# Kernel optimization log

Hardware: AMD Instinct MI355X
Metric: run time of the kernel (lower is better)

## Reference

```python
import jax, jax.numpy as jnp
import numpy as np
from jax import lax

FEAT_STRIDE = 16
SCALES = (8, 16, 32)
RATIOS = (0.5, 1.0, 2.0)
PRE_NMS = 6000
POST_NMS = 300
NMS_THRESH = 0.7
MIN_SIZE = 16.0


def _base_anchors():
    base = 16.0
    cx = cy = base / 2.0
    anchors = []
    for r in RATIOS:
        for s in SCALES:
            h = base * s * np.sqrt(r)
            w = base * s * np.sqrt(1.0 / r)
            anchors.append([cx - w / 2, cy - h / 2, cx + w / 2, cy + h / 2])
    return np.asarray(anchors, np.float32)  # [A,4] (x1,y1,x2,y2)


def _shifted_anchors(h, w):
    base = _base_anchors()
    sy = np.arange(h, dtype=np.float32) * FEAT_STRIDE
    sx = np.arange(w, dtype=np.float32) * FEAT_STRIDE
    yy, xx = np.meshgrid(sy, sx, indexing='ij')  # h-major then w, matching NHWC permute
    shifts = np.stack([xx, yy, xx, yy], axis=-1).reshape(-1, 1, 4)
    return (shifts + base[None]).reshape(-1, 4).astype(np.float32)  # [h*w*A,4]


def _conv(x, w, b, pad):
    y = lax.conv_general_dilated(x, w, (1, 1), [(pad, pad), (pad, pad)],
                                 dimension_numbers=('NCHW', 'OIHW', 'NCHW'))
    return y + b[None, :, None, None]


def _iou(box, boxes):
    lt = jnp.maximum(box[:2], boxes[:, :2])
    rb = jnp.minimum(box[2:], boxes[:, 2:])
    wh = jnp.maximum(rb - lt, 0.0)
    inter = wh[:, 0] * wh[:, 1]
    a1 = (box[2] - box[0]) * (box[3] - box[1])
    a2 = (boxes[:, 2] - boxes[:, 0]) * (boxes[:, 3] - boxes[:, 1])
    return inter / (a1 + a2 - inter + 1e-9)


def _nms_proposals(boxes, scores):
    # boxes [K,4], scores [K] -> [POST_NMS,4]
    ws = boxes[:, 2] - boxes[:, 0]
    hs = boxes[:, 3] - boxes[:, 1]
    scores = jnp.where((ws >= MIN_SIZE) & (hs >= MIN_SIZE), scores, -jnp.inf)
    top_s, idx = lax.top_k(scores, PRE_NMS)
    b = boxes[idx]

    def body(i, st):
        keep, s = st
        j = jnp.argmax(s).astype(jnp.int32)
        keep = keep.at[i].set(j)
        sup = _iou(b[j], b) >= NMS_THRESH  # suppresses j itself too (iou=1)
        s = jnp.where(sup, -jnp.inf, s)
        return keep, s

    keep, _ = lax.fori_loop(0, POST_NMS, body,
                            (jnp.zeros((POST_NMS,), jnp.int32), top_s))
    return b[keep]


def setup_inputs() -> dict:
    key = jax.random.key(0)
    ks = jax.random.split(key, 5)
    n, c, h, w = 8, 512, 50, 64
    A = len(SCALES) * len(RATIOS)
    x = jax.random.normal(ks[0], (n, c, h, w), jnp.float32)
    w1 = jax.random.normal(ks[1], (512, 512, 3, 3), jnp.float32) * 0.02
    b1 = jnp.zeros((512,), jnp.float32)
    w_cls = jax.random.normal(ks[2], (A * 2, 512, 1, 1), jnp.float32) * 0.02
    b_cls = jnp.zeros((A * 2,), jnp.float32)
    w_bbox = jax.random.normal(ks[3], (A * 4, 512, 1, 1), jnp.float32) * 0.005
    b_bbox = jnp.zeros((A * 4,), jnp.float32)
    return {'x': x, 'w1': w1, 'b1': b1, 'w_cls': w_cls, 'b_cls': b_cls,
            'w_bbox': w_bbox, 'b_bbox': b_bbox}


def reference(x, w1, b1, w_cls, b_cls, w_bbox, b_bbox):
    n, _, h, w = x.shape
    A = len(SCALES) * len(RATIOS)
    img_h, img_w = h * FEAT_STRIDE, w * FEAT_STRIDE
    anchors = jnp.asarray(_shifted_anchors(h, w))  # [h*w*A,4]

    feat = jax.nn.relu(_conv(x, w1, b1, 1))
    cls = _conv(feat, w_cls, b_cls, 0).transpose(0, 2, 3, 1).reshape(n, h, w, A, 2)
    fg = jax.nn.softmax(cls, axis=-1)[..., 1].reshape(n, -1)  # [n, h*w*A]
    deltas = _conv(feat, w_bbox, b_bbox, 0).transpose(0, 2, 3, 1).reshape(n, -1, 4)

    # decode deltas against anchors
    aw = anchors[:, 2] - anchors[:, 0]
    ah = anchors[:, 3] - anchors[:, 1]
    acx = anchors[:, 0] + 0.5 * aw
    acy = anchors[:, 1] + 0.5 * ah
    cx = deltas[..., 0] * aw + acx
    cy = deltas[..., 1] * ah + acy
    pw = jnp.exp(deltas[..., 2]) * aw
    ph = jnp.exp(deltas[..., 3]) * ah
    boxes = jnp.stack([cx - 0.5 * pw, cy - 0.5 * ph,
                       cx + 0.5 * pw, cy + 0.5 * ph], axis=-1)  # [n,K,4]
    hi = jnp.asarray([img_w, img_h, img_w, img_h], jnp.float32)
    boxes = jnp.clip(boxes, 0.0, hi)

    rois = jax.vmap(_nms_proposals)(boxes, fg)  # [n,POST_NMS,4]
    roi_indices = jnp.repeat(jnp.arange(n, dtype=jnp.int32), POST_NMS)
    return rois.reshape(-1, 4), roi_indices
```

## Files before the change

kernel.cpp:

```cpp
#include <hip/hip_runtime.h>
#include <math.h>

#define NIMG 8
#define CIN  512
#define HF   50
#define WF   64
#define HW   3200
#define NA   9
#define KPER 28800
#define PRE  6000
#define POST 300

#define WHT_ELEMS  32768

#define NW    94
#define NCAP  6016
#define NTRI  4465

#define XTROWS 52
#define XTCOLS 66
#define XT_ELEMS ((size_t)NIMG * XTROWS * XTCOLS * CIN)
#define XT_BYTES (XT_ELEMS * 2)

#define WPK_ELEMS ((size_t)2 * 4 * 9 * 16 * 4096)
#define WPK_HALF  (4 * 9 * 16 * 4096)

#define SCALE_X 256.0f
#define SCALE_W 16384.0f
#define INV_SCALE (1.0f / 4194304.0f)

#define PB_XT   1600
#define PB_HALO 64
#define PB_WPK  288
#define PB_PH   16
#define PB_TOT  (PB_XT + PB_HALO + PB_WPK + PB_PH)

#define HALO_VPI 14848
#define HALO_TOT (NIMG * HALO_VPI)

typedef _Float16 f16x8 __attribute__((ext_vector_type(8)));
typedef float f32x4  __attribute__((ext_vector_type(4)));
typedef unsigned short u16x8 __attribute__((ext_vector_type(8)));
typedef unsigned long long u64;

__constant__ float BASEA[9][4] = {
  {-82.509667991878083f, -37.254833995939042f,  98.509667991878083f,  53.254833995939042f},
  {-173.01933598375617f, -82.509667991878083f, 189.01933598375617f,   98.509667991878083f},
  {-354.03867196751233f, -173.01933598375617f, 370.03867196751233f,  189.01933598375617f},
  { -56.0f,  -56.0f,  72.0f,  72.0f},
  {-120.0f, -120.0f, 136.0f, 136.0f},
  {-248.0f, -248.0f, 264.0f, 264.0f},
  {-37.254833995939042f, -82.509667991878083f,  53.254833995939042f,  98.509667991878083f},
  {-82.509667991878083f, -173.01933598375617f,  98.509667991878083f, 189.01933598375617f},
  {-173.01933598375617f, -354.03867196751233f, 189.01933598375617f,  370.03867196751233f},
};

__device__ __forceinline__ unsigned int ordf(float f) {
  unsigned int u = __float_as_uint(f);
  return (u & 0x80000000u) ? ~u : (u | 0x80000000u);
}

__device__ __forceinline__ unsigned short f2h(float f) {
  union { _Float16 h; unsigned short u; } cv;
  cv.h = (_Float16)f;
  return cv.u;
}
__device__ __forceinline__ float h2f(unsigned short u) {
  union { _Float16 h; unsigned short u; } cv;
  cv.u = u;
  return (float)cv.h;
}

__global__ __launch_bounds__(256) void k_prep_all(
    const float4* __restrict__ x4,
    const float* __restrict__ w1,
    const float* __restrict__ wc, const float* __restrict__ bc,
    const float* __restrict__ wb, const float* __restrict__ bb,
    unsigned short* __restrict__ xh, unsigned short* __restrict__ xl,
    unsigned short* __restrict__ wpk,
    float* __restrict__ WHT2, float* __restrict__ bh) {
  __shared__ float tile[128][65];
  const int blk = blockIdx.x;
  const int t = threadIdx.x;

  if (blk < PB_XT) {
    const int cic = blk & 3;
    const int rest = blk >> 2;
    const int hrow = rest % 50;
    const int n = rest / 50;
#pragma unroll
    for (int jj = 0; jj < 8; ++jj) {
      const int e = t + 256 * jj;
      const int row = e >> 4, c4 = e & 15;
      const float4 v = x4[(((size_t)(n * CIN + cic * 128 + row) * HF + hrow) << 4) + c4];
      tile[row][c4 * 4 + 0] = v.x;
      tile[row][c4 * 4 + 1] = v.y;
      tile[row][c4 * 4 + 2] = v.z;
      tile[row][c4 * 4 + 3] = v.w;
    }
    __syncthreads();
#pragma unroll
    for (int jj = 0; jj < 4; ++jj) {
      const int e = t + 256 * jj;
      const int w = e >> 4, c8 = e & 15;
      const size_t base = ((size_t)((n * XTROWS + (hrow + 1)) * XTCOLS) + (w + 1)) * CIN
                          + cic * 128 + c8 * 8;
      u16x8 hv, lv;
#pragma unroll
      for (int u = 0; u < 8; ++u) {
        const float g = tile[c8 * 8 + u][w] * SCALE_X;
        const unsigned short hh = f2h(g);
        hv[u] = (short)hh;
        lv[u] = (short)f2h(g - h2f(hh));
      }
      *reinterpret_cast<u16x8*>(xh + base) = hv;
      *reinterpret_cast<u16x8*>(xl + base) = lv;
    }
  } else if (blk < PB_XT + PB_HALO) {
    const u16x8 z = {0, 0, 0, 0, 0, 0, 0, 0};
    const int tid = (blk - PB_XT) * 256 + t;
    for (int v = tid; v < HALO_TOT; v += PB_HALO * 256) {
      const int n = v / HALO_VPI;
      const int r = v - n * HALO_VPI;
      int row, col, v8;
      if (r < 8448) {
        row = (r < 4224) ? 0 : 51;
        const int r2 = (r < 4224) ? r : r - 4224;
        col = r2 >> 6;
        v8 = r2 & 63;
      } else {
        const int q = r - 8448;
        row = 1 + (q >> 7);
        const int rr = q & 127;
        col = (rr >= 64) ? 65 : 0;
        v8 = rr & 63;
      }
      const size_t off = ((size_t)((n * XTROWS + row) * XTCOLS) + col) * CIN + v8 * 8;
      *reinterpret_cast<u16x8*>(xh + off) = z;
      *reinterpret_cast<u16x8*>(xl + off) = z;
    }
  } else if (blk < PB_XT + PB_HALO + PB_WPK) {
    const int tot = (int)WPK_ELEMS;
    const int tid = (blk - PB_XT - PB_HALO) * 256 + t;
    for (int idx = tid; idx < tot; idx += PB_WPK * 256) {
      const int i = idx & 4095;
      int rest = idx >> 12;
      const int ks = rest & 15; rest >>= 4;
      const int tap = rest % 9; rest /= 9;
      const int cob = rest & 3;
      const int sp = rest >> 2;
      const int col = i >> 5;
      const int slotp = (i >> 3) & 3;
      const int j = i & 7;
      const int s = slotp ^ ((col >> 1) & 3);
      const int ci = ks * 32 + s * 8 + j;
      const int co = cob * 128 + col;
      const float g = w1[((size_t)co * CIN + ci) * 9 + tap] * SCALE_W;
      const unsigned short hh = f2h(g);
      wpk[idx] = sp ? f2h(g - h2f(hh)) : hh;
    }
  } else {
    const int TOT = WHT_ELEMS + 64;
    const int tid = (blk - PB_XT - PB_HALO - PB_WPK) * 256 + t;
    for (int idx = tid; idx < TOT; idx += PB_PH * 256) {
      if (idx < WHT_ELEMS) {
        int r = idx & 3;
        int o = (idx >> 2) & 63;
        int c = (idx >> 8) * 4 + r;
        float v = 0.0f;
        if (o < 18) v = wc[(size_t)o * CIN + c];
        else if (o < 54) v = wb[(size_t)(o - 18) * CIN + c];
        WHT2[idx] = v;
      } else {
        int o = idx - WHT_ELEMS;
        float v = 0.0f;
        if (o < 18) v = bc[o];
        else if (o < 54) v = bb[o - 18];
        bh[o] = v;
      }
    }
  }
}

#define GLDS(gp, lp) __builtin_amdgcn_global_load_lds( \
    (const __attribute__((address_space(1))) unsigned int*)(gp), \
    (__attribute__((address_space(3))) unsigned int*)(lp), 16, 0, 0)

__global__ __launch_bounds__(256, 2) void k_convmfma(
    const unsigned short* __restrict__ xh,
    const unsigned short* __restrict__ xl,
    const unsigned short* __restrict__ wpk,
    const float* __restrict__ b1,
    float* __restrict__ feat) {
  __shared__ unsigned short lds[2][4][4096];

  const int raw = blockIdx.x;
  const int xcd = raw & 7;
  const int idx = raw >> 3;
  const int cob = xcd >> 1;
  const int pb  = (xcd & 1) * 100 + idx;

  const int n   = pb / 25;
  const int h0  = (pb - n * 25) * 2;
  const int t   = threadIdx.x;
  const int wid = t >> 6;
  const int l   = t & 63;
  const int wm  = wid >> 1;
  const int wn  = wid & 1;

  const int colp = l >> 2;
  const int sB = (((l & 3) ^ ((l >> 3) & 3)) << 3);
  const unsigned short* xsrc = (wid == 3) ? xl : xh;
  const size_t wA_base = (size_t)(wid & 1) * WPK_HALF;

  const int fr = l & 15;
  const int fq = l >> 4;
  const int slotr = ((fq ^ ((fr >> 1) & 3)) << 4);

  f32x4 acc[4][4] = {};

  auto stage = [&](int sbuf, int ti) {
    const int ks  = ti / 9;
    const int tap = ti - ks * 9;
    if (wid < 2) {
      const unsigned short* gp = wpk + wA_base
          + ((size_t)((cob * 9 + tap) * 16 + ks) << 12) + l * 8;
      unsigned short* lp = &lds[sbuf][wid][0];
#pragma unroll
      for (int q = 0; q < 8; ++q)
        GLDS(gp + q * 512, lp + q * 512);
    } else {
      const int ky = (tap * 11) >> 5;
      const int kx = tap - ky * 3;
      const size_t ebase = ((size_t)((n * XTROWS + h0 + ky) * XTCOLS + kx + colp) << 9)
                           + ks * 32 + sB;
      unsigned short* lp = &lds[sbuf][wid][0];
#pragma unroll
      for (int q = 0; q < 8; ++q)
        GLDS(xsrc + ebase + ((size_t)(((q >> 2) * XTCOLS + (q & 3) * 16)) << 9),
             lp + q * 512);
    }
  };

  stage(0, 0);
  __syncthreads();

  int buf = 0;
  for (int ti = 0; ti < 144; ++ti) {
    if (ti < 143) stage(buf ^ 1, ti + 1);

    f16x8 ah[4], al[4], bhf[4], blf[4];
#pragma unroll
    for (int mi = 0; mi < 4; ++mi) {
      const int off = (((wm << 6) + (mi << 4) + fr) << 6) + slotr;
      ah[mi] = *(const f16x8*)((const char*)&lds[buf][0][0] + off);
      al[mi] = *(const f16x8*)((const char*)&lds[buf][1][0] + off);
    }
#pragma unroll
    for (int ni = 0; ni < 4; ++ni) {
      const int off = (((wn << 6) + (ni << 4) + fr) << 6) + slotr;
      bhf[ni] = *(const f16x8*)((const char*)&lds[buf][2][0] + off);
      blf[ni] = *(const f16x8*)((const char*)&lds[buf][3][0] + off);
    }
#pragma unroll
    for (int mi = 0; mi < 4; ++mi)
#pragma unroll
      for (int ni = 0; ni < 4; ++ni) {
        acc[mi][ni] = __builtin_amdgcn_mfma_f32_16x16x32_f16(ah[mi], bhf[ni], acc[mi][ni], 0, 0, 0);
        acc[mi][ni] = __builtin_amdgcn_mfma_f32_16x16x32_f16(ah[mi], blf[ni], acc[mi][ni], 0, 0, 0);
        acc[mi][ni] = __builtin_amdgcn_mfma_f32_16x16x32_f16(al[mi], bhf[ni], acc[mi][ni], 0, 0, 0);
      }
    __syncthreads();
    buf ^= 1;
  }

  const int h = h0 + wn;
#pragma unroll
  for (int mi = 0; mi < 4; ++mi) {
    const int co = (cob << 7) + (wm << 6) + (mi << 4) + (fq << 2);
    const float4 bias = *(const float4*)&b1[co];
#pragma unroll
    for (int ni = 0; ni < 4; ++ni) {
      const int w = (ni << 4) + fr;
      float4 v;
      v.x = fmaxf(fmaf(acc[mi][ni][0], INV_SCALE, bias.x), 0.0f);
      v.y = fmaxf(fmaf(acc[mi][ni][1], INV_SCALE, bias.y), 0.0f);
      v.z = fmaxf(fmaf(acc[mi][ni][2], INV_SCALE, bias.z), 0.0f);
      v.w = fmaxf(fmaf(acc[mi][ni][3], INV_SCALE, bias.w), 0.0f);
      *(float4*)(feat + (((size_t)n * HW + h * WF + w) << 9) + co) = v;
    }
  }
}

__global__ __launch_bounds__(256) void k_head(const float* __restrict__ feat,
                                              const float* __restrict__ WHT2,
                                              const float* __restrict__ bh,
                                              float* __restrict__ scores,
                                              float4* __restrict__ boxes) {
  __shared__ float fsh[16][512];
  __shared__ float vsh[16][64];
  const int t = threadIdx.x;
  const int wvid = t >> 6;
  const int o = t & 63;
  const int pos0 = blockIdx.x * 16;

  {
    const float4* fsrc = reinterpret_cast<const float4*>(feat + ((size_t)pos0 << 9));
    float4* fdst = reinterpret_cast<float4*>(&fsh[0][0]);
#pragma unroll
    for (int i = 0; i < 8; ++i) fdst[t + 256 * i] = fsrc[t + 256 * i];
  }
  __syncthreads();

  {
    const int p0 = wvid * 4;
    float a0 = 0.f, a1 = 0.f, a2 = 0.f, a3 = 0.f;
    const float4* wp = reinterpret_cast<const float4*>(WHT2);
    const float4* f0 = reinterpret_cast<const float4*>(&fsh[p0 + 0][0]);
    const float4* f1 = reinterpret_cast<const float4*>(&fsh[p0 + 1][0]);
    const float4* f2 = reinterpret_cast<const float4*>(&fsh[p0 + 2][0]);
    const float4* f3 = reinterpret_cast<const float4*>(&fsh[p0 + 3][0]);
#pragma unroll 4
    for (int c4 = 0; c4 < 128; ++c4) {
      float4 w4 = wp[c4 * 64 + o];
      float4 v;
      v = f0[c4];
      a0 = fmaf(w4.x, v.x, a0); a0 = fmaf(w4.y, v.y, a0);
      a0 = fmaf(w4.z, v.z, a0); a0 = fmaf(w4.w, v.w, a0);
      v = f1[c4];
      a1 = fmaf(w4.x, v.x, a1); a1 = fmaf(w4.y, v.y, a1);
      a1 = fmaf(w4.z, v.z, a1); a1 = fmaf(w4.w, v.w, a1);
      v = f2[c4];
      a2 = fmaf(w4.x, v.x, a2); a2 = fmaf(w4.y, v.y, a2);
      a2 = fmaf(w4.z, v.z, a2); a2 = fmaf(w4.w, v.w, a2);
      v = f3[c4];
      a3 = fmaf(w4.x, v.x, a3); a3 = fmaf(w4.y, v.y, a3);
      a3 = fmaf(w4.z, v.z, a3); a3 = fmaf(w4.w, v.w, a3);
    }
    float bv = bh[o];
    vsh[p0 + 0][o] = a0 + bv;
    vsh[p0 + 1][o] = a1 + bv;
    vsh[p0 + 2][o] = a2 + bv;
    vsh[p0 + 3][o] = a3 + bv;
  }
  __syncthreads();

  if (t < 144) {
    const int p2 = t / 9, a = t % 9;
    const int pos = pos0 + p2;
    const int n = pos / HW;
    const int r = pos - n * HW;
    const int ph = r >> 6;
    const int pw = r & 63;

    float l0 = vsh[p2][a * 2];
    float l1 = vsh[p2][a * 2 + 1];
    float m  = fmaxf(l0, l1);
    float e0 = (float)exp((double)__fsub_rn(l0, m));
    float e1 = (float)exp((double)__fsub_rn(l1, m));
    float fg = __fdiv_rn(e1, __fadd_rn(e0, e1));

    float d0 = vsh[p2][18 + a * 4 + 0];
    float d1 = vsh[p2][18 + a * 4 + 1];
    float d2 = vsh[p2][18 + a * 4 + 2];
    float d3 = vsh[p2][18 + a * 4 + 3];

    float sx = (float)(pw * 16);
    float sy = (float)(ph * 16);
    float ax1 = __fadd_rn(BASEA[a][0], sx);
    float ay1 = __fadd_rn(BASEA[a][1], sy);
    float ax2 = __fadd_rn(BASEA[a][2], sx);
    float ay2 = __fadd_rn(BASEA[a][3], sy);
    float aw = __fsub_rn(ax2, ax1);
    float ah = __fsub_rn(ay2, ay1);
    float acx = __fadd_rn(ax1, __fmul_rn(0.5f, aw));
    float acy = __fadd_rn(ay1, __fmul_rn(0.5f, ah));
    float cx = __fadd_rn(__fmul_rn(d0, aw), acx);
    float cy = __fadd_rn(__fmul_rn(d1, ah), acy);
    float pwd = __fmul_rn((float)exp((double)d2), aw);
    float phd = __fmul_rn((float)exp((double)d3), ah);
    float x1 = __fsub_rn(cx, __fmul_rn(0.5f, pwd));
    float y1 = __fsub_rn(cy, __fmul_rn(0.5f, phd));
    float x2 = __fadd_rn(cx, __fmul_rn(0.5f, pwd));
    float y2 = __fadd_rn(cy, __fmul_rn(0.5f, phd));
    x1 = fminf(fmaxf(x1, 0.0f), 1024.0f);
    x2 = fminf(fmaxf(x2, 0.0f), 1024.0f);
    y1 = fminf(fmaxf(y1, 0.0f), 800.0f);
    y2 = fminf(fmaxf(y2, 0.0f), 800.0f);
    float wsz = __fsub_rn(x2, x1);
    float hsz = __fsub_rn(y2, y1);
    float sc = (wsz >= 16.0f && hsz >= 16.0f) ? fg : -__builtin_huge_valf();

    const int idx = n * KPER + r * NA + a;
    scores[idx] = sc;
    boxes[idx] = make_float4(x1, y1, x2, y2);
  }
}

__global__ __launch_bounds__(1024) void k_select(const float* __restrict__ scores,
                                                 const float4* __restrict__ boxes,
                                                 float4* __restrict__ sbox,
                                                 u64* __restrict__ valid) {
  __shared__ u64 sk[8192];
  __shared__ unsigned int whist[16][264];
  __shared__ unsigned int histT[256];
  __shared__ unsigned int sh_selB, sh_ngt, sh_binc, sh_num;
  const int n = blockIdx.x;
  const int t = threadIdx.x;
  const int wv = t >> 6;
  const float* sc = scores + (size_t)n * KPER;
  const float4* sc4 = reinterpret_cast<const float4*>(sc);

  for (int e = t; e < 8192; e += 1024) sk[e] = 0ull;

  unsigned int prefix = 0, prefMask = 0, ngt = 0, neq = 0;
  for (int shift = 24; shift >= 0; shift -= 8) {
    for (int e = t; e < 16 * 264; e += 1024) (&whist[0][0])[e] = 0u;
    __syncthreads();
    for (int i4 = t; i4 < KPER / 4; i4 += 1024) {
      const float4 v = sc4[i4];
      unsigned int u;
      u = ordf(v.x); if ((u & prefMask) == prefix) atomicAdd(&whist[wv][(u >> shift) & 255], 1u);
      u = ordf(v.y); if ((u & prefMask) == prefix) atomicAdd(&whist[wv][(u >> shift) & 255], 1u);
      u = ordf(v.z); if ((u & prefMask) == prefix) atomicAdd(&whist[wv][(u >> shift) & 255], 1u);
      u = ordf(v.w); if ((u & prefMask) == prefix) atomicAdd(&whist[wv][(u >> shift) & 255], 1u);
    }
    __syncthreads();
    if (t < 256) {
      unsigned int s = 0;
#pragma unroll
      for (int w = 0; w < 16; ++w) s += whist[w][t];
      histT[t] = s;
    }
    __syncthreads();
    if (t == 0) {
      unsigned int cnt = ngt;
      for (int b = 255; b >= 0; --b) {
        unsigned int c = histT[b];
        if (cnt + c >= (unsigned)PRE) { sh_selB = (unsigned)b; sh_ngt = cnt; sh_binc = c; break; }
        cnt += c;
      }
    }
    __syncthreads();
    prefix |= (sh_selB << shift);
    prefMask |= (0xFFu << shift);
    ngt = sh_ngt;
    neq = sh_binc;
    __syncthreads();
  }
  const unsigned int T = prefix;
  const unsigned int needed = (unsigned)PRE - ngt;
  unsigned int J = 0xFFFFFFFFu;
  if (needed < neq) {
    if (t < 256) histT[t] = 0;
    __syncthreads();
    for (int i = t; i < KPER; i += 1024)
      if (ordf(sc[i]) == T) atomicAdd(&histT[i >> 7], 1u);
    __syncthreads();
    if (t == 0) {
      unsigned int cnt = 0;
      for (int b = 0; b < 256; ++b) {
        unsigned int c = histT[b];
        if (cnt + c >= needed) { sh_selB = (unsigned)b; sh_ngt = needed - cnt; break; }
        cnt += c;
      }
    }
    __syncthreads();
    const unsigned int selH = sh_selB;
    const unsigned int needLow = sh_ngt;
    __syncthreads();
    if (t < 128) histT[t] = 0;
    __syncthreads();
    for (int i = t; i < KPER; i += 1024)
      if (ordf(sc[i]) == T && ((unsigned)(i >> 7)) == selH) atomicAdd(&histT[i & 127], 1u);
    __syncthreads();
    if (t == 0) {
      unsigned int cnt = 0;
      for (int b = 0; b < 128; ++b) {
        unsigned int c = histT[b];
        if (cnt + c >= needLow) { sh_selB = (selH << 7) | (unsigned)b; break; }
        cnt += c;
      }
    }
    __syncthreads();
    J = sh_selB;
  }

  if (t == 0) sh_num = 0;
  __syncthreads();
  for (int i4 = t; i4 < KPER / 4; i4 += 1024) {
    const float4 v = sc4[i4];
    const float vv[4] = {v.x, v.y, v.z, v.w};
#pragma unroll
    for (int c = 0; c < 4; ++c) {
      const int i = i4 * 4 + c;
      unsigned int u = ordf(vv[c]);
      bool in = (u > T) || (u == T && (unsigned)i <= J);
      if (in) {
        unsigned int p = atomicAdd(&sh_num, 1u);
        sk[p] = (((u64)u) << 32) | (u64)(~(unsigned int)i);
      }
    }
  }
  __syncthreads();

  for (int k = 2; k <= 8192; k <<= 1) {
    for (int j = k >> 1; j > 0; j >>= 1) {
      for (int p = t; p < 4096; p += 1024) {
        const int i = ((p & ~(j - 1)) << 1) | (p & (j - 1));
        const int ip = i | j;
        u64 a = sk[i], b = sk[ip];
        const bool desc = ((i & k) == 0);
        if ((a < b) == desc) { sk[i] = b; sk[ip] = a; }
      }
      __syncthreads();
    }
  }

  for (int e = t; e < NCAP; e += 1024) {
    float4 bx = make_float4(0.f, 0.f, 0.f, 0.f);
    if (e < PRE) {
      unsigned idx = ~(unsigned)(sk[e] & 0xFFFFFFFFull);
      bx = boxes[(size_t)n * KPER + idx];
    }
    sbox[(size_t)n * NCAP + e] = bx;
  }
  if (t < 128) {
    u64 w = 0;
    if (t < NW) {
      for (int b = 0; b < 64; ++b) {
        int e = t * 64 + b;
        if (e < PRE && ((sk[e] >> 32) > 0x007FFFFFull)) w |= 1ull << b;
      }
    }
    valid[n * 128 + t] = w;
  }
}

__global__ __launch_bounds__(64) void k_mask(const float4* __restrict__ sbox,
                                             u64* __restrict__ mask) {
  const int p = blockIdx.x;
  const int n = blockIdx.y;
  int ib = (int)((189.0 - sqrt(35721.0 - 8.0 * (double)p)) * 0.5);
  while (94 * (ib + 1) - (ib * (ib + 1)) / 2 <= p) ++ib;
  while (94 * ib - ((ib - 1) * ib) / 2 > p) --ib;
  const int jb = ib + (p - (94 * ib - ((ib - 1) * ib) / 2));

  const int r = threadIdx.x;
  const int i = ib * 64 + r;
  __shared__ float4 jbox[64];
  jbox[r] = sbox[(size_t)n * NCAP + jb * 64 + r];
  __syncthreads();
  const float4 pbx = sbox[(size_t)n * NCAP + i];
  const float pa = __fmul_rn(__fsub_rn(pbx.z, pbx.x), __fsub_rn(pbx.w, pbx.y));
  u64 word = 0;
#pragma unroll 8
  for (int b = 0; b < 64; ++b) {
    const float4 q = jbox[b];
    float ltx = fmaxf(pbx.x, q.x);
    float lty = fmaxf(pbx.y, q.y);
    float rbx = fminf(pbx.z, q.z);
    float rby = fminf(pbx.w, q.w);
    float wv = fmaxf(__fsub_rn(rbx, ltx), 0.0f);
    float hv = fmaxf(__fsub_rn(rby, lty), 0.0f);
    float inter = __fmul_rn(wv, hv);
    float a2 = __fmul_rn(__fsub_rn(q.z, q.x), __fsub_rn(q.w, q.y));
    float denom = __fadd_rn(__fsub_rn(__fadd_rn(pa, a2), inter), 1e-9f);
    float iou = __fdiv_rn(inter, denom);
    if (iou >= 0.7f) word |= (1ull << b);
  }
  mask[((size_t)(n * NCAP) + i) * NW + jb] = word;
}

__global__ __launch_bounds__(64) void k_scan(const u64* __restrict__ mask,
                                             const u64* __restrict__ valid,
                                             const float4* __restrict__ sbox,
                                             float* __restrict__ out) {
  const int n = blockIdx.x;
  const int lane = threadIdx.x;
  u64 s0 = 0, s1 = 0;
  const u64 v0 = valid[n * 128 + 2 * lane];
  const u64 v1 = valid[n * 128 + 2 * lane + 1];
  const u64* mrow = mask + (size_t)n * NCAP * NW;
  __shared__ int keep_list[POST];
  int kept = 0;

  const int NG = PRE / 16;
  ulonglong2 c0[16], c1[16], c2[16];
#pragma unroll
  for (int r = 0; r < 16; ++r)
    c0[r] = ((const ulonglong2*)(mrow + (size_t)r * NW))[lane];
#pragma unroll
  for (int r = 0; r < 16; ++r)
    c1[r] = ((const ulonglong2*)(mrow + (size_t)(16 + r) * NW))[lane];

  for (int g = 0; g < NG; ++g) {
    if (kept >= POST) break;
    if (g + 2 < NG) {
#pragma unroll
      for (int r = 0; r < 16; ++r)
        c2[r] = ((const ulonglong2*)(mrow + (size_t)((g + 2) * 16 + r) * NW))[lane];
    }
#pragma unroll
    for (int r = 0; r < 16; ++r) {
      if (kept < POST) {
        const int i = g * 16 + r;
        const int w = i >> 6;
        const u64 avail = (w & 1) ? (v1 & ~s1) : (v0 & ~s0);
        const unsigned h32 = (unsigned)(avail >> (i & 32));
        const unsigned wrd = __shfl(h32, w >> 1, 64);
        if ((wrd >> (i & 31)) & 1u) {
          if (lane == 0) keep_list[kept] = i;
          ++kept;
          s0 |= c0[r].x;
          s1 |= c0[r].y;
        }
      }
    }
#pragma unroll
    for (int r = 0; r < 16; ++r) { c0[r] = c1[r]; c1[r] = c2[r]; }
  }
  __syncthreads();

  for (int it = lane; it < POST; it += 64) {
    const int cand = (it < kept) ? keep_list[it] : 0;
    const float4 b = sbox[(size_t)n * NCAP + cand];
    float* orow = out + ((size_t)n * POST + it) * 4;
    orow[0] = b.x; orow[1] = b.y; orow[2] = b.z; orow[3] = b.w;
    out[(size_t)NIMG * POST * 4 + (size_t)n * POST + it] = (float)n;
  }
}

extern "C" void kernel_launch(void* const* d_in, const int* in_sizes, int n_in,
                              void* d_out, int out_size, void* d_ws, size_t ws_size,
                              hipStream_t stream) {
  const float* x    = (const float*)d_in[0];
  const float* w1   = (const float*)d_in[1];
  const float* b1   = (const float*)d_in[2];
  const float* wcls = (const float*)d_in[3];
  const float* bcls = (const float*)d_in[4];
  const float* wbb  = (const float*)d_in[5];
  const float* bbb  = (const float*)d_in[6];
  float* out = (float*)d_out;

  char* ws = (char*)d_ws;
  size_t off = 0;
  float* feat = (float*)(ws + off);               off += (size_t)NIMG * HW * CIN * 4;
  float* scores = (float*)(ws + off);             off += (size_t)NIMG * KPER * 4;
  float4* boxes = (float4*)(ws + off);            off += (size_t)NIMG * KPER * 16;
  float4* sbox = (float4*)(ws + off);             off += (size_t)NIMG * NCAP * 16;
  u64* valid = (u64*)(ws + off);                  off += (size_t)NIMG * 128 * 8;
  u64* mask = (u64*)(ws + off);                   off += (size_t)NIMG * NCAP * NW * 8;
  float* WHT2 = (float*)(ws + off);               off += (size_t)WHT_ELEMS * 4;
  float* bh   = (float*)(ws + off);               off += 256;
  unsigned short* xTh = (unsigned short*)(ws + off); off += XT_BYTES;
  unsigned short* xTl = (unsigned short*)(ws + off); off += XT_BYTES;
  unsigned short* wpk = (unsigned short*)(ws + off); off += WPK_ELEMS * 2;

  k_prep_all<<<PB_TOT, 256, 0, stream>>>((const float4*)x, w1, wcls, bcls, wbb, bbb,
                                         xTh, xTl, wpk, WHT2, bh);
  k_convmfma<<<800, 256, 0, stream>>>(xTh, xTl, wpk, b1, feat);
  k_head<<<(NIMG * HW) / 16, 256, 0, stream>>>(feat, WHT2, bh, scores, boxes);
  k_select<<<NIMG, 1024, 0, stream>>>(scores, boxes, sbox, valid);
  k_mask<<<dim3(NTRI, NIMG), 64, 0, stream>>>(sbox, mask);
  k_scan<<<NIMG, 64, 0, stream>>>(mask, valid, sbox, out);
}
```

Measured before the change: 747.8 us.

## Share weight tiles across two pixel blocks per 512-thread conv workgroup

The conv MFMA kernel now runs 512-thread workgroups that each compute two pixel-row blocks (pb and pb+100) with one shared set of staged weight tiles. This halves the weight traffic from global memory into LDS per output. In exchange each block uses 1.5x the LDS, has more threads per block and half as many blocks (400), which may lower occupancy or latency hiding.

```diff
diff --git a/kernel.cpp b/kernel.cpp
--- a/kernel.cpp
+++ b/kernel.cpp
@@ -186,36 +186,42 @@
     (const __attribute__((address_space(1))) unsigned int*)(gp), \
     (__attribute__((address_space(3))) unsigned int*)(lp), 16, 0, 0)
 
-__global__ __launch_bounds__(256, 2) void k_convmfma(
+__global__ __launch_bounds__(512, 2) void k_convmfma(
     const unsigned short* __restrict__ xh,
     const unsigned short* __restrict__ xl,
     const unsigned short* __restrict__ wpk,
     const float* __restrict__ b1,
     float* __restrict__ feat) {
-  __shared__ unsigned short lds[2][4][4096];
+  __shared__ unsigned short lds[2][6][4096];
 
   const int raw = blockIdx.x;
   const int xcd = raw & 7;
   const int idx = raw >> 3;
   const int cob = xcd >> 1;
-  const int pb  = (xcd & 1) * 100 + idx;
-
-  const int n   = pb / 25;
-  const int h0  = (pb - n * 25) * 2;
+  const int pp  = (xcd & 1) * 50 + idx;
+  const int pb0 = pp;
+  const int pb1 = pp + 100;
+
+  const int n0 = pb0 / 25, h00 = (pb0 - n0 * 25) * 2;
+  const int n1 = pb1 / 25, h10 = (pb1 - n1 * 25) * 2;
+
   const int t   = threadIdx.x;
   const int wid = t >> 6;
   const int l   = t & 63;
-  const int wm  = wid >> 1;
-  const int wn  = wid & 1;
+  const int wm  = wid >> 2;
+  const int wn  = wid & 3;
 
   const int colp = l >> 2;
   const int sB = (((l & 3) ^ ((l >> 3) & 3)) << 3);
-  const unsigned short* xsrc = (wid == 3) ? xl : xh;
-  const size_t wA_base = (size_t)(wid & 1) * WPK_HALF;
 
   const int fr = l & 15;
   const int fq = l >> 4;
   const int slotr = ((fq ^ ((fr >> 1) & 3)) << 4);
+
+  const int bsel = (wid - 2) >> 1;
+  const unsigned short* xsrc = ((wid - 2) & 1) ? xl : xh;
+  const int bn  = bsel ? n1 : n0;
+  const int bh0 = bsel ? h10 : h00;
 
   f32x4 acc[4][4] = {};
 
@@ -223,16 +229,16 @@
     const int ks  = ti / 9;
     const int tap = ti - ks * 9;
     if (wid < 2) {
-      const unsigned short* gp = wpk + wA_base
+      const unsigned short* gp = wpk + (size_t)wid * WPK_HALF
           + ((size_t)((cob * 9 + tap) * 16 + ks) << 12) + l * 8;
       unsigned short* lp = &lds[sbuf][wid][0];
 #pragma unroll
       for (int q = 0; q < 8; ++q)
         GLDS(gp + q * 512, lp + q * 512);
-    } else {
+    } else if (wid < 6) {
       const int ky = (tap * 11) >> 5;
       const int kx = tap - ky * 3;
-      const size_t ebase = ((size_t)((n * XTROWS + h0 + ky) * XTCOLS + kx + colp) << 9)
+      const size_t ebase = ((size_t)((bn * XTROWS + bh0 + ky) * XTCOLS + kx + colp) << 9)
                            + ks * 32 + sB;
       unsigned short* lp = &lds[sbuf][wid][0];
 #pragma unroll
@@ -244,6 +250,8 @@
 
   stage(0, 0);
   __syncthreads();
+
+  const int btile = 2 + ((wn >> 1) << 1);
 
   int buf = 0;
   for (int ti = 0; ti < 144; ++ti) {
@@ -258,9 +266,9 @@
     }
 #pragma unroll
     for (int ni = 0; ni < 4; ++ni) {
-      const int off = (((wn << 6) + (ni << 4) + fr) << 6) + slotr;
-      bhf[ni] = *(const f16x8*)((const char*)&lds[buf][2][0] + off);
-      blf[ni] = *(const f16x8*)((const char*)&lds[buf][3][0] + off);
+      const int off = ((((wn & 1) << 6) + (ni << 4) + fr) << 6) + slotr;
+      bhf[ni] = *(const f16x8*)((const char*)&lds[buf][btile][0] + off);
+      blf[ni] = *(const f16x8*)((const char*)&lds[buf][btile + 1][0] + off);
     }
 #pragma unroll
     for (int mi = 0; mi < 4; ++mi)
@@ -274,7 +282,10 @@
     buf ^= 1;
   }
 
-  const int h = h0 + wn;
+  const int pbE = (wn < 2) ? pb0 : pb1;
+  const int nE  = (wn < 2) ? n0 : n1;
+  const int h   = ((wn < 2) ? h00 : h10) + (wn & 1);
+  (void)pbE;
 #pragma unroll
   for (int mi = 0; mi < 4; ++mi) {
     const int co = (cob << 7) + (wm << 6) + (mi << 4) + (fq << 2);
@@ -287,7 +298,7 @@
       v.y = fmaxf(fmaf(acc[mi][ni][1], INV_SCALE, bias.y), 0.0f);
       v.z = fmaxf(fmaf(acc[mi][ni][2], INV_SCALE, bias.z), 0.0f);
       v.w = fmaxf(fmaf(acc[mi][ni][3], INV_SCALE, bias.w), 0.0f);
-      *(float4*)(feat + (((size_t)n * HW + h * WF + w) << 9) + co) = v;
+      *(float4*)(feat + (((size_t)nE * HW + h * WF + w) << 9) + co) = v;
     }
   }
 }
@@ -659,7 +670,7 @@
 
   k_prep_all<<<PB_TOT, 256, 0, stream>>>((const float4*)x, w1, wcls, bcls, wbb, bbb,
                                          xTh, xTl, wpk, WHT2, bh);
-  k_convmfma<<<800, 256, 0, stream>>>(xTh, xTl, wpk, b1, feat);
+  k_convmfma<<<400, 512, 0, stream>>>(xTh, xTl, wpk, b1, feat);
   k_head<<<(NIMG * HW) / 16, 256, 0, stream>>>(feat, WHT2, bh, scores, boxes);
   k_select<<<NIMG, 1024, 0, stream>>>(scores, boxes, sbox, valid);
   k_mask<<<dim3(NTRI, NIMG), 64, 0, stream>>>(sbox, mask);
```

Result: faster. 724.7 us (-3.1%).
